# Optimization experiments

Measured on AMD Instinct MI355X. Metric: run time of the kernel, lower is better.

## Reference

```python
import jax, jax.numpy as jnp
import numpy as np

TOP_K = 512  # int(node_num * K) = int(2048 * 0.25)
NEG = -1.0e12
SLOPE = 0.01  # nn.LeakyReLU default negative_slope


def setup_inputs() -> dict:
    key = jax.random.key(0)
    k1, k2, k3, k4 = jax.random.split(key, 4)
    B, N, in_c, out_c, gs = 8, 2048, 128, 128, 128
    x = jax.random.normal(k1, (B, N, in_c), dtype=jnp.float32)
    W = jax.random.normal(k2, (in_c, out_c), dtype=jnp.float32) * (1.0 / np.sqrt(in_c))
    a = jax.random.normal(k3, (2 * out_c, 1), dtype=jnp.float32) * (1.0 / np.sqrt(2 * out_c))
    GL = jax.random.normal(k4, (N, gs), dtype=jnp.float32) * (1.0 / np.sqrt(gs))
    return {"x": x, "W": W, "a": a, "GL": GL}


def reference(x, W, a, GL):
    B, N, _ = x.shape
    out_c = W.shape[1]
    # learned adjacency: softmax(relu(GL GL^T)) + I  -> [N, N]
    adj = jax.nn.softmax(jax.nn.relu(GL @ GL.T), axis=-1) + jnp.eye(N, dtype=GL.dtype)
    h = x @ W  # [B, N, out_c]
    # e[b,i,j] = LeakyReLU( [h_i ; h_j] . a ) = LeakyReLU( h_i.a1 + h_j.a2 )
    # (avoids materializing the [B, N*N, 2*out_c] concat of the original)
    a1, a2 = a[:out_c, 0], a[out_c:, 0]
    e = jax.nn.leaky_relu((h @ a1)[:, :, None] + (h @ a2)[:, None, :], SLOPE)  # [B,N,N]
    att = jnp.where(adj[None] > 0, e, NEG)
    # top-k along dim=1 (rows, per column j): transpose so that axis is last
    att_t = jnp.swapaxes(att, 1, 2)  # [B, Nj, Ni]
    _, idx = jax.lax.top_k(att_t, TOP_K)  # idx: [B, Nj, TOP_K]
    b_ix = jnp.arange(B)[:, None, None]
    j_ix = jnp.arange(N)[None, :, None]
    mask_t = jnp.zeros_like(att_t).at[b_ix, j_ix, idx].set(1.0)
    mask = jnp.swapaxes(mask_t, 1, 2)  # [B, Ni, Nj]
    att = jax.nn.softmax(att * mask, axis=2)
    h_prime = jax.nn.relu(att @ h)  # [B, N, out_c]
    return jnp.swapaxes(h_prime, -2, -1)  # [B, out_c, N]
```

## Files before the change

### kernel.cpp

```cpp
#include <hip/hip_runtime.h>
#include <hip/hip_bf16.h>
#include <math.h>


#define B_ 8
#define N_ 2048
#define C_ 128
#define TOPK_ 512
#define NCH_ 64
#define CL_ 32
#define NP1_ 2050

#define H_OFF    ((size_t)0)
#define P_OFF    (H_OFF + (size_t)B_*N_*C_)
#define Q_OFF    (P_OFF + (size_t)B_*N_)
#define QS_OFF   (Q_OFF + (size_t)B_*N_)
#define US_OFF   (QS_OFF + (size_t)B_*N_)
#define VS_OFF   (US_OFF + (size_t)B_*N_)
#define SRT_OFF  (VS_OFF + (size_t)B_*N_)
#define SUS_OFF  (SRT_OFF + (size_t)B_*N_)
#define PVS_OFF  (SUS_OFF + (size_t)B_*NP1_)
#define SUL_OFF  (PVS_OFF + (size_t)B_*NP1_)
#define PVL_OFF  (SUL_OFF + (size_t)B_*N_*128)
#define TOTU_OFF (PVL_OFF + (size_t)B_*N_*128)
#define TOTV_OFF (TOTU_OFF + (size_t)B_*NCH_*128)
#define CSU_OFF  (TOTV_OFF + (size_t)B_*NCH_*128)
#define CPV_OFF  (CSU_OFF + (size_t)B_*(NCH_+1)*128)
#define MR_OFF   (CPV_OFF + (size_t)B_*(NCH_+1)*128)
#define MPART_OFF (MR_OFF + (size_t)B_*C_)
#define PTHR_OFF (MPART_OFF + (size_t)B_*32*C_)
#define ITHR_OFF (PTHR_OFF + (size_t)B_)

__device__ __forceinline__ unsigned enc_f(float f) {
  unsigned b = __float_as_uint(f);
  return b ^ ((b >> 31) ? 0xFFFFFFFFu : 0x80000000u);
}
__device__ __forceinline__ float dec_f(unsigned e) {
  unsigned b = (e & 0x80000000u) ? (e ^ 0x80000000u) : ~e;
  return __uint_as_float(b);
}
__device__ __forceinline__ unsigned long long sxor64(unsigned long long v, int m) {
  int lo = __shfl_xor((int)(unsigned)(v & 0xffffffffULL), m, 64);
  int hi = __shfl_xor((int)(unsigned)(v >> 32), m, 64);
  return (((unsigned long long)(unsigned)hi) << 32) | (unsigned)lo;
}

__global__ __launch_bounds__(256) void k_gemm(const float* __restrict__ x,
                                              const float* __restrict__ W,
                                              const float* __restrict__ a,
                                              float* __restrict__ h,
                                              float* __restrict__ p,
                                              float* __restrict__ q,
                                              float* __restrict__ mpart) {
  __shared__ float Wl[64 * 128];
  __shared__ float xl[64 * 68];
  __shared__ float a1l[128], a2l[128];
  __shared__ float redp[64][8], redq[64][8];
  const int t = threadIdx.x;
  const int r0 = blockIdx.x * 64;
  if (t < 128) { a1l[t] = a[t]; a2l[t] = a[128 + t]; }
  const int cg = t & 7, rp = t >> 3;
  const int lr0 = rp * 2, lr1 = lr0 + 1;
  float acc0[16], acc1[16];
#pragma unroll
  for (int i = 0; i < 16; ++i) { acc0[i] = 0.f; acc1[i] = 0.f; }

  for (int kc = 0; kc < 2; ++kc) {
    __syncthreads();
    const float4* W4 = (const float4*)(W + (size_t)kc * 64 * 128);
    float4* Wl4 = (float4*)Wl;
#pragma unroll
    for (int i = 0; i < 8; ++i) Wl4[t + 256 * i] = W4[t + 256 * i];
#pragma unroll
    for (int i = 0; i < 4; ++i) {
      int idx = t + 256 * i;
      int row = idx >> 4, c4i = idx & 15;
      float4 v = *(const float4*)(x + (size_t)(r0 + row) * 128 + kc * 64 + c4i * 4);
      ((float4*)xl)[row * 17 + c4i] = v;
    }
    __syncthreads();
    for (int k = 0; k < 64; ++k) {
      float xv0 = xl[lr0 * 68 + k];
      float xv1 = xl[lr1 * 68 + k];
      const float4* Wr = (const float4*)(Wl + k * 128);
#pragma unroll
      for (int i = 0; i < 4; ++i) {
        float4 w = Wr[cg + 8 * i];
        acc0[i * 4 + 0] = fmaf(xv0, w.x, acc0[i * 4 + 0]);
        acc0[i * 4 + 1] = fmaf(xv0, w.y, acc0[i * 4 + 1]);
        acc0[i * 4 + 2] = fmaf(xv0, w.z, acc0[i * 4 + 2]);
        acc0[i * 4 + 3] = fmaf(xv0, w.w, acc0[i * 4 + 3]);
        acc1[i * 4 + 0] = fmaf(xv1, w.x, acc1[i * 4 + 0]);
        acc1[i * 4 + 1] = fmaf(xv1, w.y, acc1[i * 4 + 1]);
        acc1[i * 4 + 2] = fmaf(xv1, w.z, acc1[i * 4 + 2]);
        acc1[i * 4 + 3] = fmaf(xv1, w.w, acc1[i * 4 + 3]);
      }
    }
  }
  float pp0 = 0.f, qq0 = 0.f, pp1 = 0.f, qq1 = 0.f;
  size_t hb = (size_t)r0 * 128;
  __syncthreads();
  float* scratch = xl;
#pragma unroll
  for (int i = 0; i < 4; ++i) {
    int c0 = 4 * cg + 32 * i;
    float4 v0 = make_float4(acc0[i*4+0], acc0[i*4+1], acc0[i*4+2], acc0[i*4+3]);
    float4 v1 = make_float4(acc1[i*4+0], acc1[i*4+1], acc1[i*4+2], acc1[i*4+3]);
    *(float4*)(h + hb + (size_t)lr0 * 128 + c0) = v0;
    *(float4*)(h + hb + (size_t)lr1 * 128 + c0) = v1;
#pragma unroll
    for (int j = 0; j < 4; ++j) {
      int c = c0 + j;
      scratch[rp * 128 + c] = acc0[i*4+j] + acc1[i*4+j];
      pp0 = fmaf(acc0[i*4+j], a1l[c], pp0);
      qq0 = fmaf(acc0[i*4+j], a2l[c], qq0);
      pp1 = fmaf(acc1[i*4+j], a1l[c], pp1);
      qq1 = fmaf(acc1[i*4+j], a2l[c], qq1);
    }
  }
  redp[lr0][cg] = pp0; redq[lr0][cg] = qq0;
  redp[lr1][cg] = pp1; redq[lr1][cg] = qq1;
  __syncthreads();
  if (t < 64) {
    float sp = 0.f, sq = 0.f;
#pragma unroll
    for (int i = 0; i < 8; ++i) { sp += redp[t][i]; sq += redq[t][i]; }
    p[r0 + t] = sp;
    q[r0 + t] = sq;
  }
  if (t < 128) {
    float s = 0.f;
#pragma unroll
    for (int rr = 0; rr < 32; ++rr) s += scratch[rr * 128 + t];
    mpart[(size_t)blockIdx.x * 128 + t] = s;
  }
}

__global__ __launch_bounds__(1024) void k_sort(const float* __restrict__ q,
                                               const float* __restrict__ p,
                                               float* __restrict__ q_s,
                                               float* __restrict__ u_s,
                                               float* __restrict__ v_s,
                                               int* __restrict__ srt,
                                               float* __restrict__ SUS,
                                               float* __restrict__ PVS,
                                               float* __restrict__ pthr,
                                               int* __restrict__ ithr) {
  __shared__ unsigned long long sh[N_];
  __shared__ float2 sa[1024], sb[1024];
  const int blk = blockIdx.x, t = threadIdx.x;
  const bool isP = blk >= B_;
  const int b = isP ? blk - B_ : blk;
  const float* src = isP ? p : q;
  float2 f2 = *(const float2*)(src + b * N_ + 2 * t);
  unsigned k0 = enc_f(f2.x), k1 = enc_f(f2.y);
  if (isP) { k0 = ~k0; k1 = ~k1; }
  unsigned long long r0 = ((unsigned long long)k0 << 32) | (unsigned)(2 * t);
  unsigned long long r1 = ((unsigned long long)k1 << 32) | (unsigned)(2 * t + 1);

  for (int k = 2; k <= N_; k <<= 1) {
    const bool up = (((2 * t) & k) == 0);
    int j = k >> 1;
    for (; j >= 128; j >>= 1) {
      *(ulonglong2*)(sh + 2 * t) = make_ulonglong2(r0, r1);
      __syncthreads();
      int pe = (2 * t) ^ j;
      ulonglong2 pp = *(const ulonglong2*)(sh + pe);
      bool lower = (((2 * t) & j) == 0);
      bool kmin = (up == lower);
      r0 = kmin ? (r0 < pp.x ? r0 : pp.x) : (r0 > pp.x ? r0 : pp.x);
      r1 = kmin ? (r1 < pp.y ? r1 : pp.y) : (r1 > pp.y ? r1 : pp.y);
      __syncthreads();
    }
    for (; j >= 2; j >>= 1) {
      int j2 = j >> 1;
      unsigned long long p0 = sxor64(r0, j2);
      unsigned long long p1 = sxor64(r1, j2);
      bool lower = ((t & j2) == 0);
      bool kmin = (up == lower);
      r0 = kmin ? (r0 < p0 ? r0 : p0) : (r0 > p0 ? r0 : p0);
      r1 = kmin ? (r1 < p1 ? r1 : p1) : (r1 > p1 ? r1 : p1);
    }
    if (up) {
      if (r0 > r1) { unsigned long long tm = r0; r0 = r1; r1 = tm; }
    } else {
      if (r1 > r0) { unsigned long long tm = r0; r0 = r1; r1 = tm; }
    }
  }

  if (isP) {
    if (t == 255) {
      unsigned key = (unsigned)(r1 >> 32);
      pthr[b] = dec_f(~key);
      ithr[b] = (int)(unsigned)(r1 & 0xffffffffULL);
    }
    return;
  }
  float v0 = dec_f((unsigned)(r0 >> 32));
  float v1 = dec_f((unsigned)(r1 >> 32));
  int i0 = (int)(unsigned)(r0 & 0xffffffffULL);
  int i1 = (int)(unsigned)(r1 & 0xffffffffULL);
  float u0 = __expf(v0), u1 = __expf(v1);
  float w0 = __expf(0.01f * v0), w1 = __expf(0.01f * v1);
  *(float2*)(q_s + b * N_ + 2 * t) = make_float2(v0, v1);
  *(float2*)(u_s + b * N_ + 2 * t) = make_float2(u0, u1);
  *(float2*)(v_s + b * N_ + 2 * t) = make_float2(w0, w1);
  *(int2*)(srt + b * N_ + 2 * t) = make_int2(i0, i1);
  float pu = u0 + u1, pw = w0 + w1;
  sa[1023 - t].x = pu;
  sa[t].y = pw;
  __syncthreads();
  float2* cur = sa; float2* nxt = sb;
  for (int off = 1; off < 1024; off <<= 1) {
    float2 vv = cur[t];
    if (t >= off) { float2 o = cur[t - off]; vv.x += o.x; vv.y += o.y; }
    nxt[t] = vv;
    __syncthreads();
    float2* tmp = cur; cur = nxt; nxt = tmp;
  }
  float PSt = cur[1023 - t].x;
  float PPt = cur[t].y;
  *(float2*)(SUS + (size_t)b * NP1_ + 2 * t) = make_float2(PSt, PSt - u0);
  *(float2*)(PVS + (size_t)b * NP1_ + 2 * t) = make_float2(PPt - pw, PPt - w1);
  if (t == 1023) {
    SUS[(size_t)b * NP1_ + N_] = 0.f;
    PVS[(size_t)b * NP1_ + N_] = PPt;
  }
}

__global__ __launch_bounds__(256) void k_scanA(const float* __restrict__ h,
                                               const float* __restrict__ u_s,
                                               const float* __restrict__ v_s,
                                               const int* __restrict__ srt,
                                               float* __restrict__ SUl,
                                               float* __restrict__ PVl,
                                               float* __restrict__ totU,
                                               float* __restrict__ totV) {
  __shared__ float hl[2][CL_][128];
  __shared__ float ul[2][CL_], vl[2][CL_];
  __shared__ int sl[2][CL_];
  const int b = blockIdx.x >> 5, cp = blockIdx.x & 31;
  const int ch0 = cp * 2;
  const int t = threadIdx.x;
  if (t < 64) {
    int s2 = t >> 5, tt = t & 31;
    int gi = b * N_ + (ch0 + s2) * CL_ + tt;
    ul[s2][tt] = u_s[gi]; vl[s2][tt] = v_s[gi]; sl[s2][tt] = srt[gi];
  }
  __syncthreads();
  const int sub = t >> 7, c = t & 127;
  const int ch = ch0 + sub;
  const int base = b * N_ + ch * CL_;
  for (int tt = 0; tt < CL_; ++tt)
    hl[sub][tt][c] = h[((size_t)b * N_ + sl[sub][tt]) * 128 + c];
  float run = 0.f;
  for (int tt = CL_ - 1; tt >= 0; --tt) {
    run = fmaf(ul[sub][tt], hl[sub][tt][c], run);
    SUl[((size_t)(base + tt)) * 128 + c] = run;
  }
  totU[(size_t)(b * NCH_ + ch) * 128 + c] = run;
  float run2 = 0.f;
  for (int tt = 0; tt < CL_; ++tt) {
    PVl[((size_t)(base + tt)) * 128 + c] = run2;
    run2 = fmaf(vl[sub][tt], hl[sub][tt][c], run2);
  }
  totV[(size_t)(b * NCH_ + ch) * 128 + c] = run2;
}

__global__ __launch_bounds__(256) void k_fin(const float* __restrict__ totU,
                                             const float* __restrict__ totV,
                                             const float* __restrict__ mpart,
                                             float* __restrict__ CSU,
                                             float* __restrict__ CPV,
                                             float* __restrict__ mrw) {
  const int b = blockIdx.x, t = threadIdx.x;
  if (t < 128) {
    float s = 0.f;
    CSU[((size_t)(b * (NCH_ + 1) + NCH_)) * 128 + t] = 0.f;
    for (int ch = NCH_ - 1; ch >= 0; --ch) {
      s += totU[(size_t)(b * NCH_ + ch) * 128 + t];
      CSU[((size_t)(b * (NCH_ + 1) + ch)) * 128 + t] = s;
    }
    float s2 = 0.f;
    for (int ch = 0; ch < NCH_; ++ch) {
      CPV[((size_t)(b * (NCH_ + 1) + ch)) * 128 + t] = s2;
      s2 += totV[(size_t)(b * NCH_ + ch) * 128 + t];
    }
    CPV[((size_t)(b * (NCH_ + 1) + NCH_)) * 128 + t] = s2;
  } else {
    int c = t - 128;
    float s = 0.f;
    for (int j2 = 0; j2 < 32; ++j2) s += mpart[(size_t)(b * 32 + j2) * 128 + c];
    mrw[b * 128 + c] = fmaxf(s * (1.0f / (float)N_), 0.f);
  }
}

__global__ __launch_bounds__(256) void k_out(const float* __restrict__ p,
                                             const float* __restrict__ q_s,
                                             const float* __restrict__ pthr,
                                             const int* __restrict__ ithr,
                                             const float* __restrict__ SUS,
                                             const float* __restrict__ PVS,
                                             const float* __restrict__ SUl,
                                             const float* __restrict__ PVl,
                                             const float* __restrict__ CSU,
                                             const float* __restrict__ CPV,
                                             const float* __restrict__ mrw,
                                             float* __restrict__ out) {
  __shared__ float qs_l[N_];
  __shared__ float res[64 * 129];
  __shared__ float mr[128];
  __shared__ float A_s[64], B_s[64], invD[64];
  __shared__ int lo_s[64], keep_s[64];
  const int b = blockIdx.x >> 5, tile = blockIdx.x & 31;
  const int t = threadIdx.x;
  const int i0 = tile * 64;
  for (int i = t; i < N_; i += 256) qs_l[i] = q_s[b * N_ + i];
  if (t < 128) mr[t] = mrw[b * 128 + t];
  __syncthreads();
  if (t < 64) {
    float pv = p[b * N_ + i0 + t];
    float thrv = pthr[b]; int thri = ithr[b];
    bool keep = (pv > thrv) || (pv == thrv && (i0 + t) <= thri);
    keep_s[t] = keep ? 1 : 0;
    float thr = -pv;
    int lo = 0, hi = N_;
    while (lo < hi) { int mid = (lo + hi) >> 1; if (qs_l[mid] < thr) lo = mid + 1; else hi = mid; }
    lo_s[t] = lo;
    float A = __expf(pv), Bv = __expf(0.01f * pv);
    A_s[t] = A; B_s[t] = Bv;
    float sus = SUS[(size_t)b * NP1_ + lo];
    float pvs = PVS[(size_t)b * NP1_ + lo];
    invD[t] = 1.0f / fmaf(A, sus, Bv * pvs);
  }
  __syncthreads();
  const int half = t >> 7, c = t & 127;
#pragma unroll 4
  for (int ii2 = 0; ii2 < 64; ii2 += 2) {
    int ii = ii2 + half;
    float outv;
    if (keep_s[ii]) {
      int lo = lo_s[ii];
      float A = A_s[ii], Bv = B_s[ii];
      float suc, pvc;
      if (lo < N_) {
        int chn = lo >> 5;
        size_t ro = ((size_t)(b * N_ + lo)) * 128;
        size_t cu = ((size_t)(b * (NCH_ + 1))) * 128;
        suc = SUl[ro + c] + CSU[cu + (size_t)(chn + 1) * 128 + c];
        pvc = PVl[ro + c] + CPV[cu + (size_t)chn * 128 + c];
      } else {
        suc = 0.f;
        pvc = CPV[((size_t)(b * (NCH_ + 1) + NCH_)) * 128 + c];
      }
      outv = fmaxf(fmaf(A, suc, Bv * pvc) * invD[ii], 0.f);
    } else {
      outv = mr[c];
    }
    res[ii * 129 + c] = outv;
  }
  __syncthreads();
#pragma unroll
  for (int pass = 0; pass < 8; ++pass) {
    int cc = (t >> 4) + pass * 16;
    int ii4 = (t & 15) * 4;
    float4 v;
    v.x = res[(ii4 + 0) * 129 + cc];
    v.y = res[(ii4 + 1) * 129 + cc];
    v.z = res[(ii4 + 2) * 129 + cc];
    v.w = res[(ii4 + 3) * 129 + cc];
    *(float4*)(out + ((size_t)(b * C_ + cc)) * N_ + i0 + ii4) = v;
  }
}

extern "C" void kernel_launch(void* const* d_in, const int* in_sizes, int n_in,
                              void* d_out, int out_size, void* d_ws, size_t ws_size,
                              hipStream_t stream) {
  (void)in_sizes; (void)n_in; (void)out_size; (void)ws_size;
  const float* x = (const float*)d_in[0];
  const float* W = (const float*)d_in[1];
  const float* a = (const float*)d_in[2];
  float* out = (float*)d_out;
  float* ws = (float*)d_ws;

  float* h    = ws + H_OFF;
  float* p    = ws + P_OFF;
  float* q    = ws + Q_OFF;
  float* q_s  = ws + QS_OFF;
  float* u_s  = ws + US_OFF;
  float* v_s  = ws + VS_OFF;
  int*   srt  = (int*)(ws + SRT_OFF);
  float* SUS  = ws + SUS_OFF;
  float* PVS  = ws + PVS_OFF;
  float* SUl  = ws + SUL_OFF;
  float* PVl  = ws + PVL_OFF;
  float* totU = ws + TOTU_OFF;
  float* totV = ws + TOTV_OFF;
  float* CSU  = ws + CSU_OFF;
  float* CPV  = ws + CPV_OFF;
  float* mrw  = ws + MR_OFF;
  float* mpart = ws + MPART_OFF;
  float* pthr = ws + PTHR_OFF;
  int*   ithr = (int*)(ws + ITHR_OFF);

  k_gemm<<<dim3((B_ * N_) / 64), dim3(256), 0, stream>>>(x, W, a, h, p, q, mpart);
  k_sort<<<dim3(2 * B_), dim3(1024), 0, stream>>>(q, p, q_s, u_s, v_s, srt, SUS, PVS, pthr, ithr);
  k_scanA<<<dim3(B_ * NCH_ / 2), dim3(256), 0, stream>>>(h, u_s, v_s, srt, SUl, PVl, totU, totV);
  k_fin<<<dim3(B_), dim3(256), 0, stream>>>(totU, totV, mpart, CSU, CPV, mrw);
  k_out<<<dim3(B_ * 32), dim3(256), 0, stream>>>(p, q_s, pthr, ithr, SUS, PVS, SUl, PVl, CSU, CPV, mrw, out);
}
```

Baseline: 119.9 us.

## Fold chunk-prefix finalize into output kernel and reshape gemm/scan thread mapping

Removes the separate k_fin launch: each k_out block now recomputes the per-batch chunk prefix sums (CSU/CPV) and the column means in shared memory instead of reading them from global buffers. k_gemm moves to 512 threads, each computing one row instead of two. k_scanA moves to one 32-row chunk per 128-thread block with twice as many blocks. This saves a kernel launch and a global round trip. In exchange, the prefix work is done redundantly by all 32 tiles per batch, and k_out's shared-memory footprint grows substantially, which may lower occupancy.

```diff
diff --git a/kernel.cpp b/kernel.cpp
--- a/kernel.cpp
+++ b/kernel.cpp
@@ -24,10 +24,7 @@
 #define PVL_OFF  (SUL_OFF + (size_t)B_*N_*128)
 #define TOTU_OFF (PVL_OFF + (size_t)B_*N_*128)
 #define TOTV_OFF (TOTU_OFF + (size_t)B_*NCH_*128)
-#define CSU_OFF  (TOTV_OFF + (size_t)B_*NCH_*128)
-#define CPV_OFF  (CSU_OFF + (size_t)B_*(NCH_+1)*128)
-#define MR_OFF   (CPV_OFF + (size_t)B_*(NCH_+1)*128)
-#define MPART_OFF (MR_OFF + (size_t)B_*C_)
+#define MPART_OFF (TOTV_OFF + (size_t)B_*NCH_*128)
 #define PTHR_OFF (MPART_OFF + (size_t)B_*32*C_)
 #define ITHR_OFF (PTHR_OFF + (size_t)B_)
 
@@ -45,7 +42,7 @@
   return (((unsigned long long)(unsigned)hi) << 32) | (unsigned)lo;
 }
 
-__global__ __launch_bounds__(256) void k_gemm(const float* __restrict__ x,
+__global__ __launch_bounds__(512) void k_gemm(const float* __restrict__ x,
                                               const float* __restrict__ W,
                                               const float* __restrict__ a,
                                               float* __restrict__ h,
@@ -59,67 +56,56 @@
   const int t = threadIdx.x;
   const int r0 = blockIdx.x * 64;
   if (t < 128) { a1l[t] = a[t]; a2l[t] = a[128 + t]; }
-  const int cg = t & 7, rp = t >> 3;
-  const int lr0 = rp * 2, lr1 = lr0 + 1;
-  float acc0[16], acc1[16];
-#pragma unroll
-  for (int i = 0; i < 16; ++i) { acc0[i] = 0.f; acc1[i] = 0.f; }
+  const int cg = t & 7, r = t >> 3;
+  float acc[16];
+#pragma unroll
+  for (int i = 0; i < 16; ++i) acc[i] = 0.f;
 
   for (int kc = 0; kc < 2; ++kc) {
     __syncthreads();
     const float4* W4 = (const float4*)(W + (size_t)kc * 64 * 128);
     float4* Wl4 = (float4*)Wl;
 #pragma unroll
-    for (int i = 0; i < 8; ++i) Wl4[t + 256 * i] = W4[t + 256 * i];
-#pragma unroll
-    for (int i = 0; i < 4; ++i) {
-      int idx = t + 256 * i;
+    for (int i = 0; i < 4; ++i) Wl4[t + 512 * i] = W4[t + 512 * i];
+#pragma unroll
+    for (int i = 0; i < 2; ++i) {
+      int idx = t + 512 * i;
       int row = idx >> 4, c4i = idx & 15;
       float4 v = *(const float4*)(x + (size_t)(r0 + row) * 128 + kc * 64 + c4i * 4);
       ((float4*)xl)[row * 17 + c4i] = v;
     }
     __syncthreads();
     for (int k = 0; k < 64; ++k) {
-      float xv0 = xl[lr0 * 68 + k];
-      float xv1 = xl[lr1 * 68 + k];
+      float xv = xl[r * 68 + k];
       const float4* Wr = (const float4*)(Wl + k * 128);
 #pragma unroll
       for (int i = 0; i < 4; ++i) {
         float4 w = Wr[cg + 8 * i];
-        acc0[i * 4 + 0] = fmaf(xv0, w.x, acc0[i * 4 + 0]);
-        acc0[i * 4 + 1] = fmaf(xv0, w.y, acc0[i * 4 + 1]);
-        acc0[i * 4 + 2] = fmaf(xv0, w.z, acc0[i * 4 + 2]);
-        acc0[i * 4 + 3] = fmaf(xv0, w.w, acc0[i * 4 + 3]);
-        acc1[i * 4 + 0] = fmaf(xv1, w.x, acc1[i * 4 + 0]);
-        acc1[i * 4 + 1] = fmaf(xv1, w.y, acc1[i * 4 + 1]);
-        acc1[i * 4 + 2] = fmaf(xv1, w.z, acc1[i * 4 + 2]);
-        acc1[i * 4 + 3] = fmaf(xv1, w.w, acc1[i * 4 + 3]);
+        acc[i * 4 + 0] = fmaf(xv, w.x, acc[i * 4 + 0]);
+        acc[i * 4 + 1] = fmaf(xv, w.y, acc[i * 4 + 1]);
+        acc[i * 4 + 2] = fmaf(xv, w.z, acc[i * 4 + 2]);
+        acc[i * 4 + 3] = fmaf(xv, w.w, acc[i * 4 + 3]);
       }
     }
   }
-  float pp0 = 0.f, qq0 = 0.f, pp1 = 0.f, qq1 = 0.f;
+  __syncthreads();
+  float* scratch = Wl;
+  float pp = 0.f, qq = 0.f;
   size_t hb = (size_t)r0 * 128;
-  __syncthreads();
-  float* scratch = xl;
 #pragma unroll
   for (int i = 0; i < 4; ++i) {
     int c0 = 4 * cg + 32 * i;
-    float4 v0 = make_float4(acc0[i*4+0], acc0[i*4+1], acc0[i*4+2], acc0[i*4+3]);
-    float4 v1 = make_float4(acc1[i*4+0], acc1[i*4+1], acc1[i*4+2], acc1[i*4+3]);
-    *(float4*)(h + hb + (size_t)lr0 * 128 + c0) = v0;
-    *(float4*)(h + hb + (size_t)lr1 * 128 + c0) = v1;
+    float4 v0 = make_float4(acc[i*4+0], acc[i*4+1], acc[i*4+2], acc[i*4+3]);
+    *(float4*)(h + hb + (size_t)r * 128 + c0) = v0;
+    *(float4*)(scratch + r * 128 + c0) = v0;
 #pragma unroll
     for (int j = 0; j < 4; ++j) {
       int c = c0 + j;
-      scratch[rp * 128 + c] = acc0[i*4+j] + acc1[i*4+j];
-      pp0 = fmaf(acc0[i*4+j], a1l[c], pp0);
-      qq0 = fmaf(acc0[i*4+j], a2l[c], qq0);
-      pp1 = fmaf(acc1[i*4+j], a1l[c], pp1);
-      qq1 = fmaf(acc1[i*4+j], a2l[c], qq1);
-    }
-  }
-  redp[lr0][cg] = pp0; redq[lr0][cg] = qq0;
-  redp[lr1][cg] = pp1; redq[lr1][cg] = qq1;
+      pp = fmaf(acc[i*4+j], a1l[c], pp);
+      qq = fmaf(acc[i*4+j], a2l[c], qq);
+    }
+  }
+  redp[r][cg] = pp; redq[r][cg] = qq;
   __syncthreads();
   if (t < 64) {
     float sp = 0.f, sq = 0.f;
@@ -131,7 +117,7 @@
   if (t < 128) {
     float s = 0.f;
 #pragma unroll
-    for (int rr = 0; rr < 32; ++rr) s += scratch[rr * 128 + t];
+    for (int rr = 0; rr < 64; ++rr) s += scratch[rr * 128 + t];
     mpart[(size_t)blockIdx.x * 128 + t] = s;
   }
 }
@@ -228,7 +214,7 @@
   }
 }
 
-__global__ __launch_bounds__(256) void k_scanA(const float* __restrict__ h,
+__global__ __launch_bounds__(128) void k_scanA(const float* __restrict__ h,
                                                const float* __restrict__ u_s,
                                                const float* __restrict__ v_s,
                                                const int* __restrict__ srt,
@@ -236,63 +222,29 @@
                                                float* __restrict__ PVl,
                                                float* __restrict__ totU,
                                                float* __restrict__ totV) {
-  __shared__ float hl[2][CL_][128];
-  __shared__ float ul[2][CL_], vl[2][CL_];
-  __shared__ int sl[2][CL_];
-  const int b = blockIdx.x >> 5, cp = blockIdx.x & 31;
-  const int ch0 = cp * 2;
+  __shared__ float hl[CL_][128];
+  __shared__ float ul[CL_], vl[CL_];
+  __shared__ int sl[CL_];
+  const int b = blockIdx.x >> 6, ch = blockIdx.x & 63;
   const int t = threadIdx.x;
-  if (t < 64) {
-    int s2 = t >> 5, tt = t & 31;
-    int gi = b * N_ + (ch0 + s2) * CL_ + tt;
-    ul[s2][tt] = u_s[gi]; vl[s2][tt] = v_s[gi]; sl[s2][tt] = srt[gi];
-  }
-  __syncthreads();
-  const int sub = t >> 7, c = t & 127;
-  const int ch = ch0 + sub;
   const int base = b * N_ + ch * CL_;
+  if (t < CL_) { ul[t] = u_s[base + t]; vl[t] = v_s[base + t]; sl[t] = srt[base + t]; }
+  __syncthreads();
+  const int c = t;
   for (int tt = 0; tt < CL_; ++tt)
-    hl[sub][tt][c] = h[((size_t)b * N_ + sl[sub][tt]) * 128 + c];
+    hl[tt][c] = h[((size_t)b * N_ + sl[tt]) * 128 + c];
   float run = 0.f;
   for (int tt = CL_ - 1; tt >= 0; --tt) {
-    run = fmaf(ul[sub][tt], hl[sub][tt][c], run);
+    run = fmaf(ul[tt], hl[tt][c], run);
     SUl[((size_t)(base + tt)) * 128 + c] = run;
   }
   totU[(size_t)(b * NCH_ + ch) * 128 + c] = run;
   float run2 = 0.f;
   for (int tt = 0; tt < CL_; ++tt) {
     PVl[((size_t)(base + tt)) * 128 + c] = run2;
-    run2 = fmaf(vl[sub][tt], hl[sub][tt][c], run2);
+    run2 = fmaf(vl[tt], hl[tt][c], run2);
   }
   totV[(size_t)(b * NCH_ + ch) * 128 + c] = run2;
-}
-
-__global__ __launch_bounds__(256) void k_fin(const float* __restrict__ totU,
-                                             const float* __restrict__ totV,
-                                             const float* __restrict__ mpart,
-                                             float* __restrict__ CSU,
-                                             float* __restrict__ CPV,
-                                             float* __restrict__ mrw) {
-  const int b = blockIdx.x, t = threadIdx.x;
-  if (t < 128) {
-    float s = 0.f;
-    CSU[((size_t)(b * (NCH_ + 1) + NCH_)) * 128 + t] = 0.f;
-    for (int ch = NCH_ - 1; ch >= 0; --ch) {
-      s += totU[(size_t)(b * NCH_ + ch) * 128 + t];
-      CSU[((size_t)(b * (NCH_ + 1) + ch)) * 128 + t] = s;
-    }
-    float s2 = 0.f;
-    for (int ch = 0; ch < NCH_; ++ch) {
-      CPV[((size_t)(b * (NCH_ + 1) + ch)) * 128 + t] = s2;
-      s2 += totV[(size_t)(b * NCH_ + ch) * 128 + t];
-    }
-    CPV[((size_t)(b * (NCH_ + 1) + NCH_)) * 128 + t] = s2;
-  } else {
-    int c = t - 128;
-    float s = 0.f;
-    for (int j2 = 0; j2 < 32; ++j2) s += mpart[(size_t)(b * 32 + j2) * 128 + c];
-    mrw[b * 128 + c] = fmaxf(s * (1.0f / (float)N_), 0.f);
-  }
 }
 
 __global__ __launch_bounds__(256) void k_out(const float* __restrict__ p,
@@ -303,12 +255,14 @@
                                              const float* __restrict__ PVS,
                                              const float* __restrict__ SUl,
                                              const float* __restrict__ PVl,
-                                             const float* __restrict__ CSU,
-                                             const float* __restrict__ CPV,
-                                             const float* __restrict__ mrw,
+                                             const float* __restrict__ totU,
+                                             const float* __restrict__ totV,
+                                             const float* __restrict__ mpart,
                                              float* __restrict__ out) {
   __shared__ float qs_l[N_];
   __shared__ float res[64 * 129];
+  __shared__ float CSUs[(NCH_ + 1) * 128];
+  __shared__ float CPVs[(NCH_ + 1) * 128];
   __shared__ float mr[128];
   __shared__ float A_s[64], B_s[64], invD[64];
   __shared__ int lo_s[64], keep_s[64];
@@ -316,7 +270,26 @@
   const int t = threadIdx.x;
   const int i0 = tile * 64;
   for (int i = t; i < N_; i += 256) qs_l[i] = q_s[b * N_ + i];
-  if (t < 128) mr[t] = mrw[b * 128 + t];
+  if (t < 128) {
+    const int c = t;
+    float s = 0.f;
+    CSUs[NCH_ * 128 + c] = 0.f;
+    for (int ch = NCH_ - 1; ch >= 0; --ch) {
+      s += totU[(size_t)(b * NCH_ + ch) * 128 + c];
+      CSUs[ch * 128 + c] = s;
+    }
+    float s2 = 0.f;
+    for (int ch = 0; ch < NCH_; ++ch) {
+      CPVs[ch * 128 + c] = s2;
+      s2 += totV[(size_t)(b * NCH_ + ch) * 128 + c];
+    }
+    CPVs[NCH_ * 128 + c] = s2;
+  } else {
+    const int c = t - 128;
+    float s = 0.f;
+    for (int j2 = 0; j2 < 32; ++j2) s += mpart[(size_t)(b * 32 + j2) * 128 + c];
+    mr[c] = fmaxf(s * (1.0f / (float)N_), 0.f);
+  }
   __syncthreads();
   if (t < 64) {
     float pv = p[b * N_ + i0 + t];
@@ -346,12 +319,11 @@
       if (lo < N_) {
         int chn = lo >> 5;
         size_t ro = ((size_t)(b * N_ + lo)) * 128;
-        size_t cu = ((size_t)(b * (NCH_ + 1))) * 128;
-        suc = SUl[ro + c] + CSU[cu + (size_t)(chn + 1) * 128 + c];
-        pvc = PVl[ro + c] + CPV[cu + (size_t)chn * 128 + c];
+        suc = SUl[ro + c] + CSUs[(chn + 1) * 128 + c];
+        pvc = PVl[ro + c] + CPVs[chn * 128 + c];
       } else {
         suc = 0.f;
-        pvc = CPV[((size_t)(b * (NCH_ + 1) + NCH_)) * 128 + c];
+        pvc = CPVs[NCH_ * 128 + c];
       }
       outv = fmaxf(fmaf(A, suc, Bv * pvc) * invD[ii], 0.f);
     } else {
@@ -396,16 +368,12 @@
   float* PVl  = ws + PVL_OFF;
   float* totU = ws + TOTU_OFF;
   float* totV = ws + TOTV_OFF;
-  float* CSU  = ws + CSU_OFF;
-  float* CPV  = ws + CPV_OFF;
-  float* mrw  = ws + MR_OFF;
   float* mpart = ws + MPART_OFF;
   float* pthr = ws + PTHR_OFF;
   int*   ithr = (int*)(ws + ITHR_OFF);
 
-  k_gemm<<<dim3((B_ * N_) / 64), dim3(256), 0, stream>>>(x, W, a, h, p, q, mpart);
+  k_gemm<<<dim3((B_ * N_) / 64), dim3(512), 0, stream>>>(x, W, a, h, p, q, mpart);
   k_sort<<<dim3(2 * B_), dim3(1024), 0, stream>>>(q, p, q_s, u_s, v_s, srt, SUS, PVS, pthr, ithr);
-  k_scanA<<<dim3(B_ * NCH_ / 2), dim3(256), 0, stream>>>(h, u_s, v_s, srt, SUl, PVl, totU, totV);
-  k_fin<<<dim3(B_), dim3(256), 0, stream>>>(totU, totV, mpart, CSU, CPV, mrw);
-  k_out<<<dim3(B_ * 32), dim3(256), 0, stream>>>(p, q_s, pthr, ithr, SUS, PVS, SUl, PVl, CSU, CPV, mrw, out);
-}
+  k_scanA<<<dim3(B_ * NCH_), dim3(128), 0, stream>>>(h, u_s, v_s, srt, SUl, PVl, totU, totV);
+  k_out<<<dim3(B_ * 32), dim3(256), 0, stream>>>(p, q_s, pthr, ithr, SUS, PVS, SUl, PVl, totU, totV, mpart, out);
+}
```

Result: slower. 131.0 us (+9.3%).

## Precompute attention scores via W·a and overlap sort with GEMM in one launch

Applied to the files above, without the earlier changes.

A new prep kernel computes p and q directly as x·(W·a1) and x·(W·a2) in double precision, so the sort no longer has to wait for the full GEMM. The GEMM blocks and the sort blocks are merged into one launch, so the 16 sort blocks run alongside the GEMM tiles. The sort itself is rewritten for 256 threads holding 8 keys each, using register sorting networks and fewer shared-memory stages. The cost is an extra launch that reads x again, double-precision arithmetic in that prep pass, and sort blocks that have lower parallelism and share resources with the GEMM blocks.

```diff
diff --git a/kernel.cpp b/kernel.cpp
--- a/kernel.cpp
+++ b/kernel.cpp
@@ -9,7 +9,7 @@
 #define TOPK_ 512
 #define NCH_ 64
 #define CL_ 32
-#define NP1_ 2050
+#define NP1_ 2052
 
 #define H_OFF    ((size_t)0)
 #define P_OFF    (H_OFF + (size_t)B_*N_*C_)
@@ -44,187 +44,252 @@
   int hi = __shfl_xor((int)(unsigned)(v >> 32), m, 64);
   return (((unsigned long long)(unsigned)hi) << 32) | (unsigned)lo;
 }
-
-__global__ __launch_bounds__(256) void k_gemm(const float* __restrict__ x,
+#define CSWAP(A, Bx, ASC) do { \
+  bool sw_ = (ASC) ? ((A) > (Bx)) : ((A) < (Bx)); \
+  if (sw_) { unsigned long long tm_ = (A); (A) = (Bx); (Bx) = tm_; } \
+} while (0)
+
+__global__ __launch_bounds__(256) void k_prep(const float* __restrict__ x,
                                               const float* __restrict__ W,
                                               const float* __restrict__ a,
+                                              float* __restrict__ p,
+                                              float* __restrict__ q) {
+  __shared__ float a1l[128], a2l[128];
+  __shared__ double wa1d[128], wa2d[128];
+  const int t = threadIdx.x;
+  if (t < 128) a1l[t] = a[t]; else a2l[t - 128] = a[t];
+  __syncthreads();
+  if (t < 128) {
+    const float* Wr = W + (size_t)t * 128;
+    double s1 = 0.0, s2 = 0.0;
+    for (int c = 0; c < 128; ++c) {
+      double wv = (double)Wr[c];
+      s1 += wv * (double)a1l[c];
+      s2 += wv * (double)a2l[c];
+    }
+    wa1d[t] = s1; wa2d[t] = s2;
+  }
+  __syncthreads();
+  const int row = blockIdx.x * 256 + t;
+  const float4* xr4 = (const float4*)(x + (size_t)row * 128);
+  double sp = 0.0, sq = 0.0;
+  for (int k4 = 0; k4 < 32; ++k4) {
+    float4 xv = xr4[k4];
+    sp += (double)xv.x * wa1d[4*k4+0] + (double)xv.y * wa1d[4*k4+1]
+        + (double)xv.z * wa1d[4*k4+2] + (double)xv.w * wa1d[4*k4+3];
+    sq += (double)xv.x * wa2d[4*k4+0] + (double)xv.y * wa2d[4*k4+1]
+        + (double)xv.z * wa2d[4*k4+2] + (double)xv.w * wa2d[4*k4+3];
+  }
+  p[row] = (float)sp;
+  q[row] = (float)sq;
+}
+
+__global__ __launch_bounds__(256) void k_mega(const float* __restrict__ x,
+                                              const float* __restrict__ W,
+                                              const float* __restrict__ p,
+                                              const float* __restrict__ q,
                                               float* __restrict__ h,
-                                              float* __restrict__ p,
-                                              float* __restrict__ q,
-                                              float* __restrict__ mpart) {
+                                              float* __restrict__ mpart,
+                                              float* __restrict__ q_s,
+                                              float* __restrict__ u_s,
+                                              float* __restrict__ v_s,
+                                              int* __restrict__ srt,
+                                              float* __restrict__ SUS,
+                                              float* __restrict__ PVS,
+                                              float* __restrict__ pthr,
+                                              int* __restrict__ ithr) {
   __shared__ float Wl[64 * 128];
   __shared__ float xl[64 * 68];
-  __shared__ float a1l[128], a2l[128];
-  __shared__ float redp[64][8], redq[64][8];
+  __shared__ unsigned long long shS[N_];
+  __shared__ float2 sa[256], sb[256];
   const int t = threadIdx.x;
-  const int r0 = blockIdx.x * 64;
-  if (t < 128) { a1l[t] = a[t]; a2l[t] = a[128 + t]; }
-  const int cg = t & 7, rp = t >> 3;
-  const int lr0 = rp * 2, lr1 = lr0 + 1;
-  float acc0[16], acc1[16];
-#pragma unroll
-  for (int i = 0; i < 16; ++i) { acc0[i] = 0.f; acc1[i] = 0.f; }
-
-  for (int kc = 0; kc < 2; ++kc) {
+
+  if (blockIdx.x < (B_ * N_) / 64) {
+    const int r0 = blockIdx.x * 64;
+    const int cg = t & 7, rp = t >> 3;
+    const int lr0 = rp * 2, lr1 = lr0 + 1;
+    float acc0[16], acc1[16];
+#pragma unroll
+    for (int i = 0; i < 16; ++i) { acc0[i] = 0.f; acc1[i] = 0.f; }
+    for (int kc = 0; kc < 2; ++kc) {
+      __syncthreads();
+      const float4* W4 = (const float4*)(W + (size_t)kc * 64 * 128);
+      float4* Wl4 = (float4*)Wl;
+#pragma unroll
+      for (int i = 0; i < 8; ++i) Wl4[t + 256 * i] = W4[t + 256 * i];
+#pragma unroll
+      for (int i = 0; i < 4; ++i) {
+        int idx = t + 256 * i;
+        int row = idx >> 4, c4i = idx & 15;
+        float4 v = *(const float4*)(x + (size_t)(r0 + row) * 128 + kc * 64 + c4i * 4);
+        ((float4*)xl)[row * 17 + c4i] = v;
+      }
+      __syncthreads();
+      for (int k = 0; k < 64; ++k) {
+        float xv0 = xl[lr0 * 68 + k];
+        float xv1 = xl[lr1 * 68 + k];
+        const float4* Wr = (const float4*)(Wl + k * 128);
+#pragma unroll
+        for (int i = 0; i < 4; ++i) {
+          float4 w = Wr[cg + 8 * i];
+          acc0[i*4+0] = fmaf(xv0, w.x, acc0[i*4+0]);
+          acc0[i*4+1] = fmaf(xv0, w.y, acc0[i*4+1]);
+          acc0[i*4+2] = fmaf(xv0, w.z, acc0[i*4+2]);
+          acc0[i*4+3] = fmaf(xv0, w.w, acc0[i*4+3]);
+          acc1[i*4+0] = fmaf(xv1, w.x, acc1[i*4+0]);
+          acc1[i*4+1] = fmaf(xv1, w.y, acc1[i*4+1]);
+          acc1[i*4+2] = fmaf(xv1, w.z, acc1[i*4+2]);
+          acc1[i*4+3] = fmaf(xv1, w.w, acc1[i*4+3]);
+        }
+      }
+    }
     __syncthreads();
-    const float4* W4 = (const float4*)(W + (size_t)kc * 64 * 128);
-    float4* Wl4 = (float4*)Wl;
-#pragma unroll
-    for (int i = 0; i < 8; ++i) Wl4[t + 256 * i] = W4[t + 256 * i];
+    float* scratch = xl;
+    size_t hb = (size_t)r0 * 128;
 #pragma unroll
     for (int i = 0; i < 4; ++i) {
-      int idx = t + 256 * i;
-      int row = idx >> 4, c4i = idx & 15;
-      float4 v = *(const float4*)(x + (size_t)(r0 + row) * 128 + kc * 64 + c4i * 4);
-      ((float4*)xl)[row * 17 + c4i] = v;
+      int c0 = 4 * cg + 32 * i;
+      float4 v0 = make_float4(acc0[i*4+0], acc0[i*4+1], acc0[i*4+2], acc0[i*4+3]);
+      float4 v1 = make_float4(acc1[i*4+0], acc1[i*4+1], acc1[i*4+2], acc1[i*4+3]);
+      *(float4*)(h + hb + (size_t)lr0 * 128 + c0) = v0;
+      *(float4*)(h + hb + (size_t)lr1 * 128 + c0) = v1;
+#pragma unroll
+      for (int j = 0; j < 4; ++j)
+        scratch[rp * 128 + c0 + j] = acc0[i*4+j] + acc1[i*4+j];
     }
     __syncthreads();
-    for (int k = 0; k < 64; ++k) {
-      float xv0 = xl[lr0 * 68 + k];
-      float xv1 = xl[lr1 * 68 + k];
-      const float4* Wr = (const float4*)(Wl + k * 128);
-#pragma unroll
-      for (int i = 0; i < 4; ++i) {
-        float4 w = Wr[cg + 8 * i];
-        acc0[i * 4 + 0] = fmaf(xv0, w.x, acc0[i * 4 + 0]);
-        acc0[i * 4 + 1] = fmaf(xv0, w.y, acc0[i * 4 + 1]);
-        acc0[i * 4 + 2] = fmaf(xv0, w.z, acc0[i * 4 + 2]);
-        acc0[i * 4 + 3] = fmaf(xv0, w.w, acc0[i * 4 + 3]);
-        acc1[i * 4 + 0] = fmaf(xv1, w.x, acc1[i * 4 + 0]);
-        acc1[i * 4 + 1] = fmaf(xv1, w.y, acc1[i * 4 + 1]);
-        acc1[i * 4 + 2] = fmaf(xv1, w.z, acc1[i * 4 + 2]);
-        acc1[i * 4 + 3] = fmaf(xv1, w.w, acc1[i * 4 + 3]);
+    if (t < 128) {
+      float s = 0.f;
+#pragma unroll
+      for (int rr = 0; rr < 32; ++rr) s += scratch[rr * 128 + t];
+      mpart[(size_t)blockIdx.x * 128 + t] = s;
+    }
+    return;
+  }
+
+  const int sblk = blockIdx.x - (B_ * N_) / 64;
+  const bool isP = sblk >= B_;
+  const int b = isP ? sblk - B_ : sblk;
+  const float* src = isP ? p : q;
+  unsigned long long r[8];
+  {
+    float4 f0 = *(const float4*)(src + b * N_ + 8 * t);
+    float4 f1 = *(const float4*)(src + b * N_ + 8 * t + 4);
+    float vs[8] = {f0.x, f0.y, f0.z, f0.w, f1.x, f1.y, f1.z, f1.w};
+#pragma unroll
+    for (int s = 0; s < 8; ++s) {
+      unsigned kk = enc_f(vs[s]);
+      if (isP) kk = ~kk;
+      r[s] = (((unsigned long long)kk) << 32) | (unsigned)(8 * t + s);
+    }
+  }
+  CSWAP(r[0], r[1], true);  CSWAP(r[2], r[3], false);
+  CSWAP(r[4], r[5], true);  CSWAP(r[6], r[7], false);
+  CSWAP(r[0], r[2], true);  CSWAP(r[1], r[3], true);
+  CSWAP(r[4], r[6], false); CSWAP(r[5], r[7], false);
+  CSWAP(r[0], r[1], true);  CSWAP(r[2], r[3], true);
+  CSWAP(r[4], r[5], false); CSWAP(r[6], r[7], false);
+  {
+    const bool u8 = ((t & 1) == 0);
+    CSWAP(r[0], r[4], u8); CSWAP(r[1], r[5], u8);
+    CSWAP(r[2], r[6], u8); CSWAP(r[3], r[7], u8);
+    CSWAP(r[0], r[2], u8); CSWAP(r[1], r[3], u8);
+    CSWAP(r[4], r[6], u8); CSWAP(r[5], r[7], u8);
+    CSWAP(r[0], r[1], u8); CSWAP(r[2], r[3], u8);
+    CSWAP(r[4], r[5], u8); CSWAP(r[6], r[7], u8);
+  }
+  for (int k = 16; k <= N_; k <<= 1) {
+    const bool up = ((t & (k >> 3)) == 0);
+    for (int j = k >> 1; j >= 8; j >>= 1) {
+      const int m = j >> 3;
+      const bool lower = ((t & m) == 0);
+      const bool kmin = (up == lower);
+      if (m >= 64) {
+        __syncthreads();
+#pragma unroll
+        for (int s = 0; s < 8; s += 2)
+          *(ulonglong2*)(shS + 8 * t + s) = make_ulonglong2(r[s], r[s + 1]);
+        __syncthreads();
+        const int pt = t ^ m;
+#pragma unroll
+        for (int s = 0; s < 8; ++s) {
+          unsigned long long pv = shS[8 * pt + s];
+          r[s] = kmin ? (r[s] < pv ? r[s] : pv) : (r[s] > pv ? r[s] : pv);
+        }
+      } else {
+#pragma unroll
+        for (int s = 0; s < 8; ++s) {
+          unsigned long long pv = sxor64(r[s], m);
+          r[s] = kmin ? (r[s] < pv ? r[s] : pv) : (r[s] > pv ? r[s] : pv);
+        }
       }
     }
-  }
-  float pp0 = 0.f, qq0 = 0.f, pp1 = 0.f, qq1 = 0.f;
-  size_t hb = (size_t)r0 * 128;
-  __syncthreads();
-  float* scratch = xl;
-#pragma unroll
-  for (int i = 0; i < 4; ++i) {
-    int c0 = 4 * cg + 32 * i;
-    float4 v0 = make_float4(acc0[i*4+0], acc0[i*4+1], acc0[i*4+2], acc0[i*4+3]);
-    float4 v1 = make_float4(acc1[i*4+0], acc1[i*4+1], acc1[i*4+2], acc1[i*4+3]);
-    *(float4*)(h + hb + (size_t)lr0 * 128 + c0) = v0;
-    *(float4*)(h + hb + (size_t)lr1 * 128 + c0) = v1;
-#pragma unroll
-    for (int j = 0; j < 4; ++j) {
-      int c = c0 + j;
-      scratch[rp * 128 + c] = acc0[i*4+j] + acc1[i*4+j];
-      pp0 = fmaf(acc0[i*4+j], a1l[c], pp0);
-      qq0 = fmaf(acc0[i*4+j], a2l[c], qq0);
-      pp1 = fmaf(acc1[i*4+j], a1l[c], pp1);
-      qq1 = fmaf(acc1[i*4+j], a2l[c], qq1);
-    }
-  }
-  redp[lr0][cg] = pp0; redq[lr0][cg] = qq0;
-  redp[lr1][cg] = pp1; redq[lr1][cg] = qq1;
-  __syncthreads();
-  if (t < 64) {
-    float sp = 0.f, sq = 0.f;
-#pragma unroll
-    for (int i = 0; i < 8; ++i) { sp += redp[t][i]; sq += redq[t][i]; }
-    p[r0 + t] = sp;
-    q[r0 + t] = sq;
-  }
-  if (t < 128) {
-    float s = 0.f;
-#pragma unroll
-    for (int rr = 0; rr < 32; ++rr) s += scratch[rr * 128 + t];
-    mpart[(size_t)blockIdx.x * 128 + t] = s;
-  }
-}
-
-__global__ __launch_bounds__(1024) void k_sort(const float* __restrict__ q,
-                                               const float* __restrict__ p,
-                                               float* __restrict__ q_s,
-                                               float* __restrict__ u_s,
-                                               float* __restrict__ v_s,
-                                               int* __restrict__ srt,
-                                               float* __restrict__ SUS,
-                                               float* __restrict__ PVS,
-                                               float* __restrict__ pthr,
-                                               int* __restrict__ ithr) {
-  __shared__ unsigned long long sh[N_];
-  __shared__ float2 sa[1024], sb[1024];
-  const int blk = blockIdx.x, t = threadIdx.x;
-  const bool isP = blk >= B_;
-  const int b = isP ? blk - B_ : blk;
-  const float* src = isP ? p : q;
-  float2 f2 = *(const float2*)(src + b * N_ + 2 * t);
-  unsigned k0 = enc_f(f2.x), k1 = enc_f(f2.y);
-  if (isP) { k0 = ~k0; k1 = ~k1; }
-  unsigned long long r0 = ((unsigned long long)k0 << 32) | (unsigned)(2 * t);
-  unsigned long long r1 = ((unsigned long long)k1 << 32) | (unsigned)(2 * t + 1);
-
-  for (int k = 2; k <= N_; k <<= 1) {
-    const bool up = (((2 * t) & k) == 0);
-    int j = k >> 1;
-    for (; j >= 128; j >>= 1) {
-      *(ulonglong2*)(sh + 2 * t) = make_ulonglong2(r0, r1);
-      __syncthreads();
-      int pe = (2 * t) ^ j;
-      ulonglong2 pp = *(const ulonglong2*)(sh + pe);
-      bool lower = (((2 * t) & j) == 0);
-      bool kmin = (up == lower);
-      r0 = kmin ? (r0 < pp.x ? r0 : pp.x) : (r0 > pp.x ? r0 : pp.x);
-      r1 = kmin ? (r1 < pp.y ? r1 : pp.y) : (r1 > pp.y ? r1 : pp.y);
-      __syncthreads();
-    }
-    for (; j >= 2; j >>= 1) {
-      int j2 = j >> 1;
-      unsigned long long p0 = sxor64(r0, j2);
-      unsigned long long p1 = sxor64(r1, j2);
-      bool lower = ((t & j2) == 0);
-      bool kmin = (up == lower);
-      r0 = kmin ? (r0 < p0 ? r0 : p0) : (r0 > p0 ? r0 : p0);
-      r1 = kmin ? (r1 < p1 ? r1 : p1) : (r1 > p1 ? r1 : p1);
-    }
-    if (up) {
-      if (r0 > r1) { unsigned long long tm = r0; r0 = r1; r1 = tm; }
-    } else {
-      if (r1 > r0) { unsigned long long tm = r0; r0 = r1; r1 = tm; }
-    }
+    CSWAP(r[0], r[4], up); CSWAP(r[1], r[5], up);
+    CSWAP(r[2], r[6], up); CSWAP(r[3], r[7], up);
+    CSWAP(r[0], r[2], up); CSWAP(r[1], r[3], up);
+    CSWAP(r[4], r[6], up); CSWAP(r[5], r[7], up);
+    CSWAP(r[0], r[1], up); CSWAP(r[2], r[3], up);
+    CSWAP(r[4], r[5], up); CSWAP(r[6], r[7], up);
   }
 
   if (isP) {
-    if (t == 255) {
-      unsigned key = (unsigned)(r1 >> 32);
+    if (t == 63) {
+      unsigned key = (unsigned)(r[7] >> 32);
       pthr[b] = dec_f(~key);
-      ithr[b] = (int)(unsigned)(r1 & 0xffffffffULL);
+      ithr[b] = (int)(unsigned)(r[7] & 0xffffffffULL);
     }
     return;
   }
-  float v0 = dec_f((unsigned)(r0 >> 32));
-  float v1 = dec_f((unsigned)(r1 >> 32));
-  int i0 = (int)(unsigned)(r0 & 0xffffffffULL);
-  int i1 = (int)(unsigned)(r1 & 0xffffffffULL);
-  float u0 = __expf(v0), u1 = __expf(v1);
-  float w0 = __expf(0.01f * v0), w1 = __expf(0.01f * v1);
-  *(float2*)(q_s + b * N_ + 2 * t) = make_float2(v0, v1);
-  *(float2*)(u_s + b * N_ + 2 * t) = make_float2(u0, u1);
-  *(float2*)(v_s + b * N_ + 2 * t) = make_float2(w0, w1);
-  *(int2*)(srt + b * N_ + 2 * t) = make_int2(i0, i1);
-  float pu = u0 + u1, pw = w0 + w1;
-  sa[1023 - t].x = pu;
-  sa[t].y = pw;
+  float vd[8], ud[8], wd[8];
+  int idxs[8];
+#pragma unroll
+  for (int s = 0; s < 8; ++s) {
+    vd[s] = dec_f((unsigned)(r[s] >> 32));
+    idxs[s] = (int)(unsigned)(r[s] & 0xffffffffULL);
+    ud[s] = __expf(vd[s]);
+    wd[s] = __expf(0.01f * vd[s]);
+  }
+  const int eb = b * N_ + 8 * t;
+  *(float4*)(q_s + eb)     = make_float4(vd[0], vd[1], vd[2], vd[3]);
+  *(float4*)(q_s + eb + 4) = make_float4(vd[4], vd[5], vd[6], vd[7]);
+  *(float4*)(u_s + eb)     = make_float4(ud[0], ud[1], ud[2], ud[3]);
+  *(float4*)(u_s + eb + 4) = make_float4(ud[4], ud[5], ud[6], ud[7]);
+  *(float4*)(v_s + eb)     = make_float4(wd[0], wd[1], wd[2], wd[3]);
+  *(float4*)(v_s + eb + 4) = make_float4(wd[4], wd[5], wd[6], wd[7]);
+  *(int4*)(srt + eb)       = make_int4(idxs[0], idxs[1], idxs[2], idxs[3]);
+  *(int4*)(srt + eb + 4)   = make_int4(idxs[4], idxs[5], idxs[6], idxs[7]);
+  float pu = 0.f, pw = 0.f;
+#pragma unroll
+  for (int s = 0; s < 8; ++s) { pu += ud[s]; pw += wd[s]; }
+  sa[t] = make_float2(pu, pw);
   __syncthreads();
   float2* cur = sa; float2* nxt = sb;
-  for (int off = 1; off < 1024; off <<= 1) {
+  for (int off = 1; off < 256; off <<= 1) {
     float2 vv = cur[t];
     if (t >= off) { float2 o = cur[t - off]; vv.x += o.x; vv.y += o.y; }
     nxt[t] = vv;
     __syncthreads();
     float2* tmp = cur; cur = nxt; nxt = tmp;
   }
-  float PSt = cur[1023 - t].x;
-  float PPt = cur[t].y;
-  *(float2*)(SUS + (size_t)b * NP1_ + 2 * t) = make_float2(PSt, PSt - u0);
-  *(float2*)(PVS + (size_t)b * NP1_ + 2 * t) = make_float2(PPt - pw, PPt - w1);
-  if (t == 1023) {
+  const float Pu = cur[t].x, Pw = cur[t].y;
+  const float total_u = cur[255].x;
+  const float SUFt = total_u - (Pu - pu);
+  const float PWex = Pw - pw;
+  float outS[8], outP[8];
+  float ru = 0.f, rw = 0.f;
+#pragma unroll
+  for (int s = 0; s < 8; ++s) {
+    outS[s] = SUFt - ru;  ru += ud[s];
+    outP[s] = PWex + rw;  rw += wd[s];
+  }
+  const size_t sbase = (size_t)b * NP1_ + 8 * t;
+  *(float4*)(SUS + sbase)     = make_float4(outS[0], outS[1], outS[2], outS[3]);
+  *(float4*)(SUS + sbase + 4) = make_float4(outS[4], outS[5], outS[6], outS[7]);
+  *(float4*)(PVS + sbase)     = make_float4(outP[0], outP[1], outP[2], outP[3]);
+  *(float4*)(PVS + sbase + 4) = make_float4(outP[4], outP[5], outP[6], outP[7]);
+  if (t == 255) {
     SUS[(size_t)b * NP1_ + N_] = 0.f;
-    PVS[(size_t)b * NP1_ + N_] = PPt;
+    PVS[(size_t)b * NP1_ + N_] = Pw;
   }
 }
 
@@ -403,8 +468,9 @@
   float* pthr = ws + PTHR_OFF;
   int*   ithr = (int*)(ws + ITHR_OFF);
 
-  k_gemm<<<dim3((B_ * N_) / 64), dim3(256), 0, stream>>>(x, W, a, h, p, q, mpart);
-  k_sort<<<dim3(2 * B_), dim3(1024), 0, stream>>>(q, p, q_s, u_s, v_s, srt, SUS, PVS, pthr, ithr);
+  k_prep<<<dim3(B_ * N_ / 256), dim3(256), 0, stream>>>(x, W, a, p, q);
+  k_mega<<<dim3(B_ * N_ / 64 + 2 * B_), dim3(256), 0, stream>>>(
+      x, W, p, q, h, mpart, q_s, u_s, v_s, srt, SUS, PVS, pthr, ithr);
   k_scanA<<<dim3(B_ * NCH_ / 2), dim3(256), 0, stream>>>(h, u_s, v_s, srt, SUl, PVl, totU, totV);
   k_fin<<<dim3(B_), dim3(256), 0, stream>>>(totU, totV, mpart, CSU, CPV, mrw);
   k_out<<<dim3(B_ * 32), dim3(256), 0, stream>>>(p, q_s, pthr, ithr, SUS, PVS, SUl, PVl, CSU, CPV, mrw, out);
```

Measured after the change: 130.7 us. 9.0% more time.
